# Kernel tuning notes

Measured on AMD Instinct MI355X. Metric: run time of the kernel, lower is better.

Reference implementation:

```python
import jax, jax.numpy as jnp
import numpy as np
import math

D_MODEL = 1024
N_HEAD = 16
D_K = 64
D_V = 64
EPS = 1e-6


def setup_inputs() -> dict:
    key = jax.random.key(0)
    ks = jax.random.split(key, 10)
    B, S = 4, 2048
    inp = {
        'x_queries': jax.random.normal(ks[0], (B, S, D_MODEL), jnp.float32),
        'x_keys': jax.random.normal(ks[1], (B, S, D_MODEL), jnp.float32),
        'x_values': jax.random.normal(ks[2], (B, S, D_MODEL), jnp.float32),
        'mask': jax.random.randint(ks[3], (B, S, S), 0, 2, jnp.int32),
        # Linear(d_model, n_head*d_k, bias=False) weights stored as [in, out]
        'w_q': jax.random.normal(ks[4], (D_MODEL, N_HEAD * D_K), jnp.float32) * np.sqrt(2.0 / (D_MODEL + D_K)),
        'w_k': jax.random.normal(ks[5], (D_MODEL, N_HEAD * D_K), jnp.float32) * np.sqrt(2.0 / (D_MODEL + D_K)),
        'w_v': jax.random.normal(ks[6], (D_MODEL, N_HEAD * D_V), jnp.float32) * np.sqrt(2.0 / (D_MODEL + D_V)),
        'w_0': jax.random.normal(ks[7], (N_HEAD * D_V, D_MODEL), jnp.float32) * np.sqrt(2.0 / (N_HEAD * D_V + D_MODEL)),
        'gamma': jnp.ones((D_MODEL,), jnp.float32),
        'beta': jnp.zeros((D_MODEL,), jnp.float32),
    }
    return inp


def _layer_norm(x, gamma, beta, eps=EPS):
    # Matches the torch module: std with Bessel correction, eps added to std.
    mean = jnp.mean(x, axis=-1, keepdims=True)
    std = jnp.std(x, axis=-1, keepdims=True, ddof=1)
    return gamma * (x - mean) / (std + eps) + beta


def reference(x_queries, x_keys, x_values, mask, w_q, w_k, w_v, w_0, gamma, beta):
    B, Lq, _ = x_queries.shape
    residual = x_queries
    # Projections -> [B, L, H, D]
    Q = (x_queries @ w_q).reshape(B, Lq, N_HEAD, D_K)
    K = (x_keys @ w_k).reshape(B, x_keys.shape[1], N_HEAD, D_K)
    V = (x_values @ w_v).reshape(B, x_values.shape[1], N_HEAD, D_V)
    # Scaled dot-product attention (scores materialized as in the original bmm path)
    scores = jnp.einsum('bqhd,bkhd->bhqk', Q, K) / math.sqrt(D_K)
    # NOTE: original masked_fill uses eps (not -inf) where mask == 0
    scores = jnp.where(mask[:, None, :, :] == 0, EPS, scores)
    attn = jax.nn.softmax(scores, axis=-1)
    out = jnp.einsum('bhqk,bkhd->bqhd', attn, V).reshape(B, Lq, N_HEAD * D_V)
    out = out @ w_0
    return _layer_norm(out + residual, gamma, beta)
```

## Files before the change

kernel.cpp:

```cpp
#include <hip/hip_runtime.h>
#include <hip/hip_bf16.h>
#include <math.h>

#define DM 1024
#define NH 16
#define DK 64
#define BB 4
#define SS 2048
#define EPSV 1e-6f
#define NE ((size_t)BB * SS * DM)
#define MM ((size_t)DM * DM)
#define QSCALE 0.18033688011112042f

typedef __attribute__((ext_vector_type(8))) short short8;
typedef __attribute__((ext_vector_type(4))) short short4v;
typedef __attribute__((ext_vector_type(4))) float f32x4;

__device__ inline unsigned short f2bf(float x) {
  unsigned int u = __builtin_bit_cast(unsigned int, x);
  u += 0x7FFF + ((u >> 16) & 1);
  return (unsigned short)(u >> 16);
}
__device__ inline ushort4 f2bf4(float4 v) {
  ushort4 r;
  r.x = f2bf(v.x); r.y = f2bf(v.y); r.z = f2bf(v.z); r.w = f2bf(v.w);
  return r;
}

__device__ inline float fexp2(float x) {
#if __has_builtin(__builtin_amdgcn_exp2f)
  return __builtin_amdgcn_exp2f(x);
#else
  return exp2f(x);
#endif
}

__device__ inline unsigned cvtpk_bf16(float a, float b) {
  unsigned r;
  asm("v_cvt_pk_bf16_f32 %0, %1, %2" : "=v"(r) : "v"(a), "v"(b));
  return r;
}

__device__ inline void gl_lds16(const unsigned short* g, unsigned short* l) {
  __builtin_amdgcn_global_load_lds((const __attribute__((address_space(1))) void*)g,
                                   (__attribute__((address_space(3))) void*)l, 16, 0, 0);
}

__global__ __launch_bounds__(256) void cvt_x_k(const float* __restrict__ xq,
                                               const float* __restrict__ xk,
                                               const float* __restrict__ xv,
                                               unsigned short* __restrict__ oq,
                                               unsigned short* __restrict__ ok,
                                               unsigned short* __restrict__ ov) {
  const size_t NF4 = NE / 4;
  size_t g = (size_t)blockIdx.x * 256 + threadIdx.x;
  int t = (int)(g / NF4);
  size_t i = g - (size_t)t * NF4;
  const float* s = (t == 0) ? xq : (t == 1) ? xk : xv;
  unsigned short* d = (t == 0) ? oq : (t == 1) ? ok : ov;
  float4 v = ((const float4*)s)[i];
  ((ushort4*)d)[i] = f2bf4(v);
}

__global__ __launch_bounds__(256) void cvt_wT_k(const float* __restrict__ w0,
                                                const float* __restrict__ w1,
                                                const float* __restrict__ w2,
                                                const float* __restrict__ w3,
                                                unsigned short* __restrict__ o0,
                                                unsigned short* __restrict__ o1,
                                                unsigned short* __restrict__ o2,
                                                unsigned short* __restrict__ o3) {
  __shared__ float t[32][33];
  int z = blockIdx.z;
  const float* w = (z == 0) ? w0 : (z == 1) ? w1 : (z == 2) ? w2 : w3;
  unsigned short* o = (z == 0) ? o0 : (z == 1) ? o1 : (z == 2) ? o2 : o3;
  float sc = (z == 0) ? QSCALE : 1.0f;
  int n0 = blockIdx.x * 32, k0 = blockIdx.y * 32;
  int tx = threadIdx.x & 31, ty = threadIdx.x >> 5;
#pragma unroll
  for (int s = 0; s < 4; ++s) t[ty + s * 8][tx] = w[(size_t)(k0 + ty + s * 8) * DM + n0 + tx];
  __syncthreads();
#pragma unroll
  for (int s = 0; s < 4; ++s)
    o[(size_t)(n0 + ty + s * 8) * DM + k0 + tx] = f2bf(t[tx][ty + s * 8] * sc);
}

__global__ __launch_bounds__(256) void maskbits_k(const int* __restrict__ mask,
                                                  unsigned long long* __restrict__ bm) {
  const int total = BB * SS * (SS / 64);
  int lane = threadIdx.x & 63;
  int wid = (blockIdx.x * 256 + threadIdx.x) >> 6;
  int nw = (gridDim.x * 256) >> 6;
  for (int w = wid; w < total; w += nw) {
    int v = mask[(size_t)w * 64 + lane];
    unsigned long long bal = __ballot(v != 0);
    if (lane == 0) bm[w] = bal;
  }
}

__global__ __launch_bounds__(256) void vtrans_k(const unsigned short* __restrict__ Vb,
                                                unsigned short* __restrict__ VT) {
  __shared__ unsigned short t[64][72];
  int b = blockIdx.z, h = blockIdx.y, s0 = blockIdx.x * 64;
  int tid = threadIdx.x;
#pragma unroll
  for (int p = 0; p < 2; ++p) {
    int idx = p * 256 + tid;
    int r = idx >> 3, cch = (idx & 7) * 8;
    short8 v = *(const short8*)&Vb[((size_t)b * SS + s0 + r) * DM + h * DK + cch];
    *(short8*)&t[r][cch] = v;
  }
  __syncthreads();
#pragma unroll
  for (int p = 0; p < 2; ++p) {
    int idx = p * 256 + tid;
    int d = idx >> 3, sch = (idx & 7) * 8;
    union { short8 v; unsigned short u[8]; } pk;
#pragma unroll
    for (int j = 0; j < 8; ++j) pk.u[j] = t[sch + j][d];
    *(short8*)&VT[(((size_t)b * NH + h) * DK + d) * SS + s0 + sch] = pk.v;
  }
}

template <bool BF16OUT>
__global__ __launch_bounds__(256) void gemm_lds_k(const unsigned short* __restrict__ Abase,
                                                  const unsigned short* __restrict__ WTbase,
                                                  void* __restrict__ Cv, int M, int N, int K,
                                                  size_t zA, size_t zW, size_t zC) {
  __shared__ __align__(16) unsigned short As[128 * 32];
  __shared__ __align__(16) unsigned short Bs[128 * 32];
  const unsigned short* A = Abase + (size_t)blockIdx.z * zA;
  const unsigned short* WT = WTbase + (size_t)blockIdx.z * zW;
  int bm = blockIdx.y * 128, bn = blockIdx.x * 128;
  int tid = threadIdx.x, lane = tid & 63, w = tid >> 6;
  int quad = lane >> 4, c = lane & 15, wx = w & 1, wy = w >> 1;

  f32x4 acc[4][4];
#pragma unroll
  for (int mt = 0; mt < 4; ++mt)
#pragma unroll
    for (int nt = 0; nt < 4; ++nt)
#pragma unroll
      for (int r = 0; r < 4; ++r) acc[mt][nt][r] = 0.f;

  int srow = lane >> 2, scol = (lane & 3) * 8;
  const unsigned short* Ag = A + (size_t)(bm + w * 32 + srow) * K + scol;
  const unsigned short* Bg = WT + (size_t)(bn + w * 32 + srow) * K + scol;
  unsigned short* Al = &As[w * 32 * 32];
  unsigned short* Bl = &Bs[w * 32 * 32];

  for (int k0 = 0; k0 < K; k0 += 32) {
    gl_lds16(Ag + k0, Al);
    gl_lds16(Ag + (size_t)16 * K + k0, Al + 16 * 32);
    gl_lds16(Bg + k0, Bl);
    gl_lds16(Bg + (size_t)16 * K + k0, Bl + 16 * 32);
    __syncthreads();
    short8 af[4], bf[4];
#pragma unroll
    for (int mt = 0; mt < 4; ++mt) af[mt] = *(const short8*)&As[(wy * 64 + mt * 16 + c) * 32 + quad * 8];
#pragma unroll
    for (int nt = 0; nt < 4; ++nt) bf[nt] = *(const short8*)&Bs[(wx * 64 + nt * 16 + c) * 32 + quad * 8];
#pragma unroll
    for (int mt = 0; mt < 4; ++mt)
#pragma unroll
      for (int nt = 0; nt < 4; ++nt)
        acc[mt][nt] = __builtin_amdgcn_mfma_f32_16x16x32_bf16(af[mt], bf[nt], acc[mt][nt], 0, 0, 0);
    __syncthreads();
  }
#pragma unroll
  for (int mt = 0; mt < 4; ++mt)
#pragma unroll
    for (int nt = 0; nt < 4; ++nt)
#pragma unroll
      for (int r = 0; r < 4; ++r) {
        size_t idx = (size_t)blockIdx.z * zC +
                     (size_t)(bm + wy * 64 + mt * 16 + quad * 4 + r) * N + bn + wx * 64 + nt * 16 + c;
        if (BF16OUT)
          ((unsigned short*)Cv)[idx] = f2bf(acc[mt][nt][r]);
        else
          ((float*)Cv)[idx] = acc[mt][nt][r];
      }
}

__global__ __launch_bounds__(256) void attn_mfma_k(const unsigned short* __restrict__ Q,
                                                   const unsigned short* __restrict__ Kg,
                                                   const unsigned short* __restrict__ VT,
                                                   const unsigned long long* __restrict__ bm,
                                                   unsigned short* __restrict__ O) {
  __shared__ __align__(16) unsigned short Ks[2][64 * 64];
  __shared__ __align__(16) unsigned short Vs[2][64 * 64];
  int b = blockIdx.z, h = blockIdx.y, q0 = blockIdx.x * 64;
  int tid = threadIdx.x, lane = tid & 63, w = tid >> 6;
  int quad = lane >> 4, c = lane & 15;

  short8 qf[2];
  {
    const unsigned short* qp = Q + ((size_t)b * SS + q0 + w * 16 + c) * DM + h * DK + quad * 8;
    qf[0] = *(const short8*)qp;
    qf[1] = *(const short8*)(qp + 32);
  }
  const unsigned long long* bp = bm + ((size_t)b * SS + q0 + w * 16 + c) * (SS / 64);
  const int shq = quad * 4;

  short8 ones8;
#pragma unroll
  for (int j = 0; j < 8; ++j) ones8[j] = (short)0x3F80;

  f32x4 accO[4], lacc;
#pragma unroll
  for (int r = 0; r < 4; ++r) lacc[r] = 0.f;
#pragma unroll
  for (int dt = 0; dt < 4; ++dt)
#pragma unroll
    for (int r = 0; r < 4; ++r) accO[dt][r] = 0.f;

  int kr = tid >> 3;
  int scc = (tid & 7) ^ (kr & 7);
  const unsigned short* pK0 = Kg + ((size_t)b * SS + kr) * DM + h * DK + scc * 8;
  const unsigned short* pK1 = pK0 + (size_t)32 * DM;
  const unsigned short* pV0 = VT + (((size_t)b * NH + h) * DK + kr) * SS + scc * 8;
  const unsigned short* pV1 = pV0 + (size_t)32 * SS;

  const int kfo0 = c * 64 + ((quad ^ (c & 7)) * 8);
  const int kfo1 = c * 64 + (((4 + quad) ^ (c & 7)) * 8);
  const int vfo0 = c * 64 + ((((quad >> 1)) ^ (c & 7)) * 8) + (quad & 1) * 4;
  const int vfo1 = c * 64 + (((4 + (quad >> 1)) ^ (c & 7)) * 8) + (quad & 1) * 4;

  const int NT = SS / 64;

  gl_lds16(pK0, &Ks[0][w * 512]);
  gl_lds16(pK1, &Ks[0][2048 + w * 512]);
  gl_lds16(pV0, &Vs[0][w * 512]);
  gl_lds16(pV1, &Vs[0][2048 + w * 512]);
  pK0 += (size_t)64 * DM; pK1 += (size_t)64 * DM;
  pV0 += 64; pV1 += 64;

  auto tile = [&](int buf, int kt) {
    __syncthreads();
    if (kt + 1 < NT) {
      gl_lds16(pK0, &Ks[buf ^ 1][w * 512]);
      gl_lds16(pK1, &Ks[buf ^ 1][2048 + w * 512]);
      gl_lds16(pV0, &Vs[buf ^ 1][w * 512]);
      gl_lds16(pV1, &Vs[buf ^ 1][2048 + w * 512]);
      pK0 += (size_t)64 * DM; pK1 += (size_t)64 * DM;
      pV0 += 64; pV1 += 64;
    }

    f32x4 sacc[4];
#pragma unroll
    for (int nt = 0; nt < 4; ++nt) {
#pragma unroll
      for (int r = 0; r < 4; ++r) sacc[nt][r] = 0.f;
      short8 ka = *(const short8*)&Ks[buf][kfo0 + nt * 1024];
      short8 kb = *(const short8*)&Ks[buf][kfo1 + nt * 1024];
      sacc[nt] = __builtin_amdgcn_mfma_f32_16x16x32_bf16(ka, qf[0], sacc[nt], 0, 0, 0);
      sacc[nt] = __builtin_amdgcn_mfma_f32_16x16x32_bf16(kb, qf[1], sacc[nt], 0, 0, 0);
    }

    unsigned long long msh = bp[kt] >> shq;
    unsigned mlo = (unsigned)msh, mhi = (unsigned)(msh >> 32);
    unsigned padw[8];
#pragma unroll
    for (int nt = 0; nt < 4; ++nt) {
      unsigned msel = (nt & 2) ? mhi : mlo;
      const int bse = (nt & 1) * 16;
      float pv[4];
#pragma unroll
      for (int r = 0; r < 4; ++r) {
        float ex = fexp2(sacc[nt][r]);
        pv[r] = ((msel >> (bse + r)) & 1u) ? ex : 1.0f;
      }
      padw[nt * 2] = cvtpk_bf16(pv[0], pv[1]);
      padw[nt * 2 + 1] = cvtpk_bf16(pv[2], pv[3]);
    }

#pragma unroll
    for (int pkt = 0; pkt < 2; ++pkt) {
      union { unsigned u[4]; short8 s8; } pa;
#pragma unroll
      for (int i = 0; i < 4; ++i) pa.u[i] = padw[pkt * 4 + i];
      lacc = __builtin_amdgcn_mfma_f32_16x16x32_bf16(pa.s8, ones8, lacc, 0, 0, 0);
      const int vfo = pkt ? vfo1 : vfo0;
#pragma unroll
      for (int dt = 0; dt < 4; ++dt) {
        int e1 = vfo + dt * 1024;
        union { short4v h[2]; short8 s8; } vf;
        vf.h[0] = *(const short4v*)&Vs[buf][e1];
        vf.h[1] = *(const short4v*)&Vs[buf][e1 ^ 16];
        accO[dt] = __builtin_amdgcn_mfma_f32_16x16x32_bf16(pa.s8, vf.s8, accO[dt], 0, 0, 0);
      }
    }
  };

  for (int kt2 = 0; kt2 < NT; kt2 += 2) {
    tile(0, kt2);
    tile(1, kt2 + 1);
  }

  float inv[4];
#pragma unroll
  for (int r = 0; r < 4; ++r) inv[r] = 1.f / lacc[r];
#pragma unroll
  for (int dt = 0; dt < 4; ++dt)
#pragma unroll
    for (int r = 0; r < 4; ++r) {
      int q = q0 + w * 16 + quad * 4 + r;
      O[((size_t)b * SS + q) * DM + h * DK + dt * 16 + c] = f2bf(accO[dt][r] * inv[r]);
    }
}

__global__ __launch_bounds__(256) void ln_k(const float* __restrict__ P,
                                            const float* __restrict__ X,
                                            const float* __restrict__ gamma,
                                            const float* __restrict__ beta,
                                            float* __restrict__ out) {
  __shared__ float sm[4];
  int row = blockIdx.x, tid = threadIdx.x, w = tid >> 6;
  float4 p = ((const float4*)(P + (size_t)row * DM))[tid];
  float4 x = ((const float4*)(X + (size_t)row * DM))[tid];
  float4 v = make_float4(p.x + x.x, p.y + x.y, p.z + x.z, p.w + x.w);
  float s = (v.x + v.y) + (v.z + v.w);
#pragma unroll
  for (int off = 1; off < 64; off <<= 1) s += __shfl_xor(s, off);
  if ((tid & 63) == 0) sm[w] = s;
  __syncthreads();
  float mean = (sm[0] + sm[1] + sm[2] + sm[3]) * (1.f / DM);
  __syncthreads();
  float dx = v.x - mean, dy = v.y - mean, dz = v.z - mean, dw = v.w - mean;
  float s2 = (dx * dx + dy * dy) + (dz * dz + dw * dw);
#pragma unroll
  for (int off = 1; off < 64; off <<= 1) s2 += __shfl_xor(s2, off);
  if ((tid & 63) == 0) sm[w] = s2;
  __syncthreads();
  float var = (sm[0] + sm[1] + sm[2] + sm[3]) * (1.f / (DM - 1));
  float inv = 1.f / (sqrtf(var) + EPSV);
  float4 g = ((const float4*)gamma)[tid];
  float4 be = ((const float4*)beta)[tid];
  float4 y = make_float4(g.x * dx * inv + be.x, g.y * dy * inv + be.y,
                         g.z * dz * inv + be.z, g.w * dw * inv + be.w);
  ((float4*)(out + (size_t)row * DM))[tid] = y;
}

extern "C" void kernel_launch(void* const* d_in, const int* in_sizes, int n_in,
                              void* d_out, int out_size, void* d_ws, size_t ws_size,
                              hipStream_t stream) {
  const float* xq = (const float*)d_in[0];
  const float* xk = (const float*)d_in[1];
  const float* xv = (const float*)d_in[2];
  const int* mask = (const int*)d_in[3];
  const float* wq = (const float*)d_in[4];
  const float* wk = (const float*)d_in[5];
  const float* wv = (const float*)d_in[6];
  const float* w0 = (const float*)d_in[7];
  const float* gamma = (const float*)d_in[8];
  const float* beta = (const float*)d_in[9];
  float* out = (float*)d_out;

  unsigned short* xqb = (unsigned short*)d_ws;
  unsigned short* xkb = xqb + NE;
  unsigned short* xvb = xkb + NE;
  unsigned short* wTq = xvb + NE;
  unsigned short* wTk = wTq + MM;
  unsigned short* wTv = wTk + MM;
  unsigned short* wT0 = wTv + MM;
  unsigned short* Qb = wT0 + MM;
  unsigned short* Kb = Qb + NE;
  unsigned short* Vb = Kb + NE;
  unsigned short* AOb = Vb + NE;
  unsigned short* VTb = xvb;
  float* P = (float*)Qb;
  unsigned long long* bm = (unsigned long long*)d_out;

  const int M = BB * SS;
  cvt_x_k<<<(unsigned)(3 * (NE / 4) / 256), 256, 0, stream>>>(xq, xk, xv, xqb, xkb, xvb);
  cvt_wT_k<<<dim3(32, 32, 4), 256, 0, stream>>>(wq, wk, wv, w0, wTq, wTk, wTv, wT0);
  maskbits_k<<<256, 256, 0, stream>>>(mask, bm);
  gemm_lds_k<true><<<dim3(DM / 128, M / 128, 3), 256, 0, stream>>>(
      xqb, wTq, Qb, M, DM, DM, NE, MM, NE);
  vtrans_k<<<dim3(SS / 64, NH, BB), 256, 0, stream>>>(Vb, VTb);
  attn_mfma_k<<<dim3(SS / 64, NH, BB), 256, 0, stream>>>(Qb, Kb, VTb, bm, AOb);
  gemm_lds_k<false><<<dim3(DM / 128, M / 128, 1), 256, 0, stream>>>(
      AOb, wT0, P, M, DM, DM, 0, 0, 0);
  ln_k<<<M, 256, 0, stream>>>(P, xq, gamma, beta, out);
}
```

Before: 549.2 us.

## Pre-pack V tiles in MFMA fragment order and prefetch mask words

Replaces the V transpose kernel with a packing kernel that writes each 64x64 V tile directly in the order the attention MFMA consumes it. The attention loop can then read V fragments with one contiguous 16-byte LDS load instead of two swizzled 8-byte loads, and its global-to-LDS copy becomes fully contiguous per tile. It also loads the next tile's mask bitword one iteration early so its latency is hidden behind the QK MFMAs. The packing kernel does more complex strided LDS reads, and the packed layout must exactly match the fragment mapping.

```diff
diff --git a/kernel.cpp b/kernel.cpp
--- a/kernel.cpp
+++ b/kernel.cpp
@@ -13,7 +13,6 @@
 #define QSCALE 0.18033688011112042f
 
 typedef __attribute__((ext_vector_type(8))) short short8;
-typedef __attribute__((ext_vector_type(4))) short short4v;
 typedef __attribute__((ext_vector_type(4))) float f32x4;
 
 __device__ inline unsigned short f2bf(float x) {
@@ -98,27 +97,32 @@
   }
 }
 
-__global__ __launch_bounds__(256) void vtrans_k(const unsigned short* __restrict__ Vb,
-                                                unsigned short* __restrict__ VT) {
+__global__ __launch_bounds__(256) void vpack_k(const unsigned short* __restrict__ Vb,
+                                               unsigned short* __restrict__ VP) {
   __shared__ unsigned short t[64][72];
-  int b = blockIdx.z, h = blockIdx.y, s0 = blockIdx.x * 64;
+  int b = blockIdx.z, h = blockIdx.y, kt = blockIdx.x;
   int tid = threadIdx.x;
 #pragma unroll
   for (int p = 0; p < 2; ++p) {
     int idx = p * 256 + tid;
     int r = idx >> 3, cch = (idx & 7) * 8;
-    short8 v = *(const short8*)&Vb[((size_t)b * SS + s0 + r) * DM + h * DK + cch];
+    short8 v = *(const short8*)&Vb[((size_t)b * SS + kt * 64 + r) * DM + h * DK + cch];
     *(short8*)&t[r][cch] = v;
   }
   __syncthreads();
+  int o = tid >> 4, w0 = o & 3;
+  int dcol = (o >> 2) * 16 + ((tid & 15) >> 1) * 2 + (tid & 1);
+  unsigned short* dst =
+      VP + (((size_t)b * NH + h) * (SS / 64) + kt) * 4096 + (size_t)tid * 8;
 #pragma unroll
   for (int p = 0; p < 2; ++p) {
-    int idx = p * 256 + tid;
-    int d = idx >> 3, sch = (idx & 7) * 8;
     union { short8 v; unsigned short u[8]; } pk;
 #pragma unroll
-    for (int j = 0; j < 8; ++j) pk.u[j] = t[sch + j][d];
-    *(short8*)&VT[(((size_t)b * NH + h) * DK + d) * SS + s0 + sch] = pk.v;
+    for (int j = 0; j < 8; ++j) {
+      int srow = p * 32 + 16 * (j >> 2) + 4 * w0 + (j & 3);
+      pk.u[j] = t[srow][dcol];
+    }
+    *(short8*)&dst[p * 2048] = pk.v;
   }
 }
 
@@ -184,7 +188,7 @@
 
 __global__ __launch_bounds__(256) void attn_mfma_k(const unsigned short* __restrict__ Q,
                                                    const unsigned short* __restrict__ Kg,
-                                                   const unsigned short* __restrict__ VT,
+                                                   const unsigned short* __restrict__ VP,
                                                    const unsigned long long* __restrict__ bm,
                                                    unsigned short* __restrict__ O) {
   __shared__ __align__(16) unsigned short Ks[2][64 * 64];
@@ -218,13 +222,13 @@
   int scc = (tid & 7) ^ (kr & 7);
   const unsigned short* pK0 = Kg + ((size_t)b * SS + kr) * DM + h * DK + scc * 8;
   const unsigned short* pK1 = pK0 + (size_t)32 * DM;
-  const unsigned short* pV0 = VT + (((size_t)b * NH + h) * DK + kr) * SS + scc * 8;
-  const unsigned short* pV1 = pV0 + (size_t)32 * SS;
+  const unsigned short* pV0 =
+      VP + ((size_t)b * NH + h) * (SS / 64) * 4096 + (size_t)tid * 8;
+  const unsigned short* pV1 = pV0 + 2048;
 
   const int kfo0 = c * 64 + ((quad ^ (c & 7)) * 8);
   const int kfo1 = c * 64 + (((4 + quad) ^ (c & 7)) * 8);
-  const int vfo0 = c * 64 + ((((quad >> 1)) ^ (c & 7)) * 8) + (quad & 1) * 4;
-  const int vfo1 = c * 64 + (((4 + (quad >> 1)) ^ (c & 7)) * 8) + (quad & 1) * 4;
+  const int vfbase = quad * 128 + c * 8;
 
   const int NT = SS / 64;
 
@@ -233,7 +237,8 @@
   gl_lds16(pV0, &Vs[0][w * 512]);
   gl_lds16(pV1, &Vs[0][2048 + w * 512]);
   pK0 += (size_t)64 * DM; pK1 += (size_t)64 * DM;
-  pV0 += 64; pV1 += 64;
+  pV0 += 4096; pV1 += 4096;
+  unsigned long long mw = bp[0];
 
   auto tile = [&](int buf, int kt) {
     __syncthreads();
@@ -243,8 +248,9 @@
       gl_lds16(pV0, &Vs[buf ^ 1][w * 512]);
       gl_lds16(pV1, &Vs[buf ^ 1][2048 + w * 512]);
       pK0 += (size_t)64 * DM; pK1 += (size_t)64 * DM;
-      pV0 += 64; pV1 += 64;
-    }
+      pV0 += 4096; pV1 += 4096;
+    }
+    unsigned long long mw_next = (kt + 1 < NT) ? bp[kt + 1] : 0ull;
 
     f32x4 sacc[4];
 #pragma unroll
@@ -257,7 +263,7 @@
       sacc[nt] = __builtin_amdgcn_mfma_f32_16x16x32_bf16(kb, qf[1], sacc[nt], 0, 0, 0);
     }
 
-    unsigned long long msh = bp[kt] >> shq;
+    unsigned long long msh = mw >> shq;
     unsigned mlo = (unsigned)msh, mhi = (unsigned)(msh >> 32);
     unsigned padw[8];
 #pragma unroll
@@ -273,6 +279,7 @@
       padw[nt * 2] = cvtpk_bf16(pv[0], pv[1]);
       padw[nt * 2 + 1] = cvtpk_bf16(pv[2], pv[3]);
     }
+    mw = mw_next;
 
 #pragma unroll
     for (int pkt = 0; pkt < 2; ++pkt) {
@@ -280,14 +287,10 @@
 #pragma unroll
       for (int i = 0; i < 4; ++i) pa.u[i] = padw[pkt * 4 + i];
       lacc = __builtin_amdgcn_mfma_f32_16x16x32_bf16(pa.s8, ones8, lacc, 0, 0, 0);
-      const int vfo = pkt ? vfo1 : vfo0;
 #pragma unroll
       for (int dt = 0; dt < 4; ++dt) {
-        int e1 = vfo + dt * 1024;
-        union { short4v h[2]; short8 s8; } vf;
-        vf.h[0] = *(const short4v*)&Vs[buf][e1];
-        vf.h[1] = *(const short4v*)&Vs[buf][e1 ^ 16];
-        accO[dt] = __builtin_amdgcn_mfma_f32_16x16x32_bf16(pa.s8, vf.s8, accO[dt], 0, 0, 0);
+        short8 vf = *(const short8*)&Vs[buf][(pkt * 4 + dt) * 512 + vfbase];
+        accO[dt] = __builtin_amdgcn_mfma_f32_16x16x32_bf16(pa.s8, vf, accO[dt], 0, 0, 0);
       }
     }
   };
@@ -367,7 +370,7 @@
   unsigned short* Kb = Qb + NE;
   unsigned short* Vb = Kb + NE;
   unsigned short* AOb = Vb + NE;
-  unsigned short* VTb = xvb;
+  unsigned short* VPb = xvb;
   float* P = (float*)Qb;
   unsigned long long* bm = (unsigned long long*)d_out;
 
@@ -377,8 +380,8 @@
   maskbits_k<<<256, 256, 0, stream>>>(mask, bm);
   gemm_lds_k<true><<<dim3(DM / 128, M / 128, 3), 256, 0, stream>>>(
       xqb, wTq, Qb, M, DM, DM, NE, MM, NE);
-  vtrans_k<<<dim3(SS / 64, NH, BB), 256, 0, stream>>>(Vb, VTb);
-  attn_mfma_k<<<dim3(SS / 64, NH, BB), 256, 0, stream>>>(Qb, Kb, VTb, bm, AOb);
+  vpack_k<<<dim3(SS / 64, NH, BB), 256, 0, stream>>>(Vb, VPb);
+  attn_mfma_k<<<dim3(SS / 64, NH, BB), 256, 0, stream>>>(Qb, Kb, VPb, bm, AOb);
   gemm_lds_k<false><<<dim3(DM / 128, M / 128, 1), 256, 0, stream>>>(
       AOb, wT0, P, M, DM, DM, 0, 0, 0);
   ln_k<<<M, 256, 0, stream>>>(P, xq, gamma, beta, out);
```

After: 551.2 us. About the same (+0.4%).
